# Optimization experiments

Measured on AMD Instinct MI355X. Metric: run time of the kernel, lower is better.

## Reference

```python
import jax, jax.numpy as jnp
import numpy as np

N_NODES = 50000
N_PROP = 25000
N_EDGES = 600000
HIDDEN = 128


def setup_inputs() -> dict:
    key = jax.random.key(0)
    ks = jax.random.split(key, 8)
    prop_z = jax.random.normal(ks[0], (N_NODES, HIDDEN), dtype=jnp.float32)
    mol_z = jax.random.normal(ks[1], (N_NODES, HIDDEN), dtype=jnp.float32)
    # Linear(hidden, hidden) params (y = x @ W.T + b, torch convention)
    W = jax.random.normal(ks[2], (HIDDEN, HIDDEN), dtype=jnp.float32) / np.sqrt(HIDDEN)
    b = jax.random.normal(ks[3], (HIDDEN,), dtype=jnp.float32) * 0.01
    # edges: dst constrained to prop_nodes = [0, N_PROP) so in_edges(prop_nodes) == all edges
    parent_src = jax.random.randint(ks[4], (N_EDGES,), 0, N_NODES, dtype=jnp.int32)
    parent_dst = jax.random.randint(ks[5], (N_EDGES,), 0, N_PROP, dtype=jnp.int32)
    sibling_src = jax.random.randint(ks[6], (N_EDGES,), 0, N_NODES, dtype=jnp.int32)
    sibling_dst = jax.random.randint(ks[7], (N_EDGES,), 0, N_PROP, dtype=jnp.int32)
    prop_nodes = jnp.arange(N_PROP, dtype=jnp.int32)
    return {"prop_z": prop_z, "mol_z": mol_z, "W": W, "b": b,
            "parent_src": parent_src, "parent_dst": parent_dst,
            "sibling_src": sibling_src, "sibling_dst": sibling_dst,
            "prop_nodes": prop_nodes}


def reference(prop_z, mol_z, W, b, parent_src, parent_dst, sibling_src, sibling_dst, prop_nodes):
    n = prop_z.shape[0]
    # parent edges: gather src prop_z, sum into dst (copy_src + sum)
    parent_agg = jax.ops.segment_sum(prop_z[parent_src], parent_dst, num_segments=n)  # [N, H]
    # prop_z[prop_nodes] += relu(linear(parent_prop_z[prop_nodes]))
    upd = jax.nn.relu(parent_agg[prop_nodes] @ W.T + b)  # [P, H]
    prop_z = prop_z.at[prop_nodes].add(upd)
    # sibling edges: gather src mol_z, sum into dst, add at prop_nodes
    sibling_agg = jax.ops.segment_sum(mol_z[sibling_src], sibling_dst, num_segments=n)  # [N, H]
    prop_z = prop_z.at[prop_nodes].add(sibling_agg[prop_nodes])
    return prop_z
```

## Files before the change

kernel.cpp:

```cpp
#include <hip/hip_runtime.h>

#define HIDDEN    128
#define N_NODES_C 50000
#define N_PROP_C  25000
#define N_EDGES_C 600000
#define CAP       64
#define PULL_BLOCKS 6250
#define TAIL_BLOCKS 512
#define GEMV_BLOCKS 1024

__global__ __launch_bounds__(256) void scatter_kernel(
    const int* __restrict__ ps, const int* __restrict__ pd,
    const int* __restrict__ ss, const int* __restrict__ sd,
    int* __restrict__ posP, int* __restrict__ posS,
    int* __restrict__ binP, int* __restrict__ binS)
{
    int i = blockIdx.x * 256 + threadIdx.x;
    if (i < N_EDGES_C) {
        int d = pd[i];
        int r = atomicAdd(&posP[d], 1);
        if (r < CAP) binP[d * CAP + r] = ps[i];
    } else if (i < 2 * N_EDGES_C) {
        int j = i - N_EDGES_C;
        int d = sd[j];
        int r = atomicAdd(&posS[d], 1);
        if (r < CAP) binS[d * CAP + r] = ss[j];
    }
}

__global__ __launch_bounds__(256) void pull_tail_kernel(
    const float* __restrict__ prop_z, const float* __restrict__ mol_z,
    const int* __restrict__ binP, const int* __restrict__ cntP,
    const int* __restrict__ binS, const int* __restrict__ cntS,
    float* __restrict__ aggP, float* __restrict__ aggS,
    float* __restrict__ out)
{
    if (blockIdx.x >= PULL_BLOCKS) {
        const float4* src = (const float4*)(prop_z + (size_t)N_PROP_C * HIDDEN);
        float4*       dst = (float4*)(out + (size_t)N_PROP_C * HIDDEN);
        const int n4 = (N_NODES_C - N_PROP_C) * HIDDEN / 4;
        for (int i = (blockIdx.x - PULL_BLOCKS) * 256 + threadIdx.x; i < n4;
             i += TAIL_BLOCKS * 256)
            dst[i] = src[i];
        return;
    }
    int task = blockIdx.x * 8 + (threadIdx.x >> 5);
    int lane = threadIdx.x & 31;
    const float4* tab; const int* bin; float4* dst; int r, n;
    if (task < N_PROP_C) {
        r = task;            tab = (const float4*)prop_z;
        bin = binP + r * CAP; n = min(cntP[r], CAP); dst = (float4*)aggP;
    } else {
        r = task - N_PROP_C; tab = (const float4*)mol_z;
        bin = binS + r * CAP; n = min(cntS[r], CAP); dst = (float4*)aggS;
    }
    float4 acc = make_float4(0.f, 0.f, 0.f, 0.f);
    int i = 0;
    for (; i + 4 <= n; i += 4) {
        int s0 = bin[i], s1 = bin[i + 1], s2 = bin[i + 2], s3 = bin[i + 3];
        float4 a = tab[s0 * 32 + lane];
        float4 b = tab[s1 * 32 + lane];
        float4 c = tab[s2 * 32 + lane];
        float4 d = tab[s3 * 32 + lane];
        acc.x += (a.x + b.x) + (c.x + d.x);
        acc.y += (a.y + b.y) + (c.y + d.y);
        acc.z += (a.z + b.z) + (c.z + d.z);
        acc.w += (a.w + b.w) + (c.w + d.w);
    }
    for (; i < n; ++i) {
        float4 a = tab[bin[i] * 32 + lane];
        acc.x += a.x; acc.y += a.y; acc.z += a.z; acc.w += a.w;
    }
    dst[r * 32 + lane] = acc;
}

__global__ __launch_bounds__(256) void gemv_out_kernel(
    const float* __restrict__ prop_z,
    const float* __restrict__ aggP, const float* __restrict__ aggS,
    const float* __restrict__ W, const float* __restrict__ bias,
    float* __restrict__ out)
{
    __shared__ float4 Wl[HIDDEN * 32];
    __shared__ float  rowP[8][HIDDEN];
    __shared__ float  rowS[8][HIDDEN];

    const float4* W4 = (const float4*)W;
    for (int i = threadIdx.x; i < HIDDEN * 32; i += 256) {
        int c = i >> 5, k4 = i & 31;
        Wl[(c << 5) | (k4 ^ (c & 31))] = W4[i];
    }
    const int t    = threadIdx.x;
    const int g    = t >> 5;
    const int l4   = t & 31;
    const int c    = t & 127;
    const int half = t >> 7;
    const float bc = bias[c];
    __syncthreads();

    for (int base = blockIdx.x * 8; base < N_PROP_C; base += GEMV_BLOCKS * 8) {
        ((float4*)rowP[g])[l4] = ((const float4*)aggP)[(base + g) * 32 + l4];
        ((float4*)rowS[g])[l4] = ((const float4*)aggS)[(base + g) * 32 + l4];
        __syncthreads();

        const int r0 = half * 4;
        float a0 = bc, a1 = bc, a2 = bc, a3 = bc;
        #pragma unroll
        for (int k4i = 0; k4i < 32; ++k4i) {
            float4 w  = Wl[(c << 5) | (k4i ^ (c & 31))];
            float4 p0 = ((const float4*)rowP[r0 + 0])[k4i];
            float4 p1 = ((const float4*)rowP[r0 + 1])[k4i];
            float4 p2 = ((const float4*)rowP[r0 + 2])[k4i];
            float4 p3 = ((const float4*)rowP[r0 + 3])[k4i];
            a0 = fmaf(w.x, p0.x, fmaf(w.y, p0.y, fmaf(w.z, p0.z, fmaf(w.w, p0.w, a0))));
            a1 = fmaf(w.x, p1.x, fmaf(w.y, p1.y, fmaf(w.z, p1.z, fmaf(w.w, p1.w, a1))));
            a2 = fmaf(w.x, p2.x, fmaf(w.y, p2.y, fmaf(w.z, p2.z, fmaf(w.w, p2.w, a2))));
            a3 = fmaf(w.x, p3.x, fmaf(w.y, p3.y, fmaf(w.z, p3.z, fmaf(w.w, p3.w, a3))));
        }
        float acc[4] = {a0, a1, a2, a3};
        #pragma unroll
        for (int j = 0; j < 4; ++j) {
            int row = base + r0 + j;
            out[(size_t)row * HIDDEN + c] =
                prop_z[(size_t)row * HIDDEN + c] + fmaxf(acc[j], 0.0f)
                + rowS[r0 + j][c];
        }
        __syncthreads();
    }
}

extern "C" void kernel_launch(void* const* d_in, const int* in_sizes, int n_in,
                              void* d_out, int out_size, void* d_ws, size_t ws_size,
                              hipStream_t stream)
{
    const float* prop_z      = (const float*)d_in[0];
    const float* mol_z       = (const float*)d_in[1];
    const float* W           = (const float*)d_in[2];
    const float* b           = (const float*)d_in[3];
    const int*   parent_src  = (const int*)d_in[4];
    const int*   parent_dst  = (const int*)d_in[5];
    const int*   sibling_src = (const int*)d_in[6];
    const int*   sibling_dst = (const int*)d_in[7];

    float* out = (float*)d_out;

    int*   binP = (int*)d_ws;
    int*   binS = binP + (size_t)N_PROP_C * CAP;
    int*   posP = binS + (size_t)N_PROP_C * CAP;
    int*   posS = posP + N_PROP_C;
    float* aggP = (float*)(posS + N_PROP_C);
    float* aggS = aggP + (size_t)N_PROP_C * HIDDEN;

    hipMemsetAsync(posP, 0, 2 * N_PROP_C * sizeof(int), stream);

    int blocks_2e = (2 * N_EDGES_C + 255) / 256;
    scatter_kernel<<<blocks_2e, 256, 0, stream>>>(parent_src, parent_dst,
                                                  sibling_src, sibling_dst,
                                                  posP, posS, binP, binS);

    pull_tail_kernel<<<PULL_BLOCKS + TAIL_BLOCKS, 256, 0, stream>>>(
        prop_z, mol_z, binP, posP, binS, posS, aggP, aggS, out);

    gemv_out_kernel<<<GEMV_BLOCKS, 256, 0, stream>>>(
        prop_z, aggP, aggS, W, b, out);
}
```

Measured before the change: 284.9 us.

## Replace FP32 GEMV epilogue with bf16 MFMA matmul and bf16 parent aggregates

The parent aggregation now stores its result as bf16 instead of fp32. The linear layer is computed with 16x16x32 bf16 MFMA instructions, using W converted to bf16 and held in swizzled shared memory, in place of the scalar FMA GEMV. The pull loop also gains an 8-way unrolled gather to keep more loads in flight. This cuts ALU work and aggregate traffic, at the cost of bf16 rounding error in the matmul inputs, and each block still converts W redundantly.

```diff
diff --git a/kernel.cpp b/kernel.cpp
--- a/kernel.cpp
+++ b/kernel.cpp
@@ -7,7 +7,16 @@
 #define CAP       64
 #define PULL_BLOCKS 6250
 #define TAIL_BLOCKS 512
-#define GEMV_BLOCKS 1024
+#define MFMA_BLOCKS 391
+
+typedef __attribute__((ext_vector_type(8))) short short8;
+typedef __attribute__((ext_vector_type(4))) float f32x4;
+
+__device__ __forceinline__ unsigned short f2bf(float x) {
+    unsigned u = __float_as_uint(x);
+    u += 0x7fffu + ((u >> 16) & 1u);
+    return (unsigned short)(u >> 16);
+}
 
 __global__ __launch_bounds__(256) void scatter_kernel(
     const int* __restrict__ ps, const int* __restrict__ pd,
@@ -32,7 +41,7 @@
     const float* __restrict__ prop_z, const float* __restrict__ mol_z,
     const int* __restrict__ binP, const int* __restrict__ cntP,
     const int* __restrict__ binS, const int* __restrict__ cntS,
-    float* __restrict__ aggP, float* __restrict__ aggS,
+    short* __restrict__ aggPb, float* __restrict__ aggS,
     float* __restrict__ out)
 {
     if (blockIdx.x >= PULL_BLOCKS) {
@@ -46,16 +55,33 @@
     }
     int task = blockIdx.x * 8 + (threadIdx.x >> 5);
     int lane = threadIdx.x & 31;
-    const float4* tab; const int* bin; float4* dst; int r, n;
-    if (task < N_PROP_C) {
+    const float4* tab; const int* bin; int r, n;
+    bool parent = task < N_PROP_C;
+    if (parent) {
         r = task;            tab = (const float4*)prop_z;
-        bin = binP + r * CAP; n = min(cntP[r], CAP); dst = (float4*)aggP;
+        bin = binP + r * CAP; n = min(cntP[r], CAP);
     } else {
         r = task - N_PROP_C; tab = (const float4*)mol_z;
-        bin = binS + r * CAP; n = min(cntS[r], CAP); dst = (float4*)aggS;
+        bin = binS + r * CAP; n = min(cntS[r], CAP);
     }
     float4 acc = make_float4(0.f, 0.f, 0.f, 0.f);
     int i = 0;
+    for (; i + 8 <= n; i += 8) {
+        int s0 = bin[i],     s1 = bin[i + 1], s2 = bin[i + 2], s3 = bin[i + 3];
+        int s4 = bin[i + 4], s5 = bin[i + 5], s6 = bin[i + 6], s7 = bin[i + 7];
+        float4 a = tab[s0 * 32 + lane];
+        float4 b = tab[s1 * 32 + lane];
+        float4 c = tab[s2 * 32 + lane];
+        float4 d = tab[s3 * 32 + lane];
+        float4 e = tab[s4 * 32 + lane];
+        float4 f = tab[s5 * 32 + lane];
+        float4 g = tab[s6 * 32 + lane];
+        float4 h = tab[s7 * 32 + lane];
+        acc.x += ((a.x + b.x) + (c.x + d.x)) + ((e.x + f.x) + (g.x + h.x));
+        acc.y += ((a.y + b.y) + (c.y + d.y)) + ((e.y + f.y) + (g.y + h.y));
+        acc.z += ((a.z + b.z) + (c.z + d.z)) + ((e.z + f.z) + (g.z + h.z));
+        acc.w += ((a.w + b.w) + (c.w + d.w)) + ((e.w + f.w) + (g.w + h.w));
+    }
     for (; i + 4 <= n; i += 4) {
         int s0 = bin[i], s1 = bin[i + 1], s2 = bin[i + 2], s3 = bin[i + 3];
         float4 a = tab[s0 * 32 + lane];
@@ -71,60 +97,72 @@
         float4 a = tab[bin[i] * 32 + lane];
         acc.x += a.x; acc.y += a.y; acc.z += a.z; acc.w += a.w;
     }
-    dst[r * 32 + lane] = acc;
-}
-
-__global__ __launch_bounds__(256) void gemv_out_kernel(
+    if (parent) {
+        ushort4 p;
+        p.x = f2bf(acc.x); p.y = f2bf(acc.y); p.z = f2bf(acc.z); p.w = f2bf(acc.w);
+        *(ushort4*)(aggPb + (size_t)r * HIDDEN + lane * 4) = p;
+    } else {
+        ((float4*)aggS)[r * 32 + lane] = acc;
+    }
+}
+
+__global__ __launch_bounds__(256) void mfma_out_kernel(
     const float* __restrict__ prop_z,
-    const float* __restrict__ aggP, const float* __restrict__ aggS,
+    const short* __restrict__ aggPb, const float* __restrict__ aggS,
     const float* __restrict__ W, const float* __restrict__ bias,
     float* __restrict__ out)
 {
-    __shared__ float4 Wl[HIDDEN * 32];
-    __shared__ float  rowP[8][HIDDEN];
-    __shared__ float  rowS[8][HIDDEN];
+    __shared__ __align__(16) short Wb[HIDDEN * HIDDEN];
 
     const float4* W4 = (const float4*)W;
-    for (int i = threadIdx.x; i < HIDDEN * 32; i += 256) {
-        int c = i >> 5, k4 = i & 31;
-        Wl[(c << 5) | (k4 ^ (c & 31))] = W4[i];
-    }
-    const int t    = threadIdx.x;
-    const int g    = t >> 5;
-    const int l4   = t & 31;
-    const int c    = t & 127;
-    const int half = t >> 7;
-    const float bc = bias[c];
+    for (int ch = threadIdx.x; ch < HIDDEN * HIDDEN / 8; ch += 256) {
+        int c = ch >> 4, kb = ch & 15;
+        float4 w0 = W4[ch * 2], w1 = W4[ch * 2 + 1];
+        short8 s;
+        s[0] = (short)f2bf(w0.x); s[1] = (short)f2bf(w0.y);
+        s[2] = (short)f2bf(w0.z); s[3] = (short)f2bf(w0.w);
+        s[4] = (short)f2bf(w1.x); s[5] = (short)f2bf(w1.y);
+        s[6] = (short)f2bf(w1.z); s[7] = (short)f2bf(w1.w);
+        ((short8*)Wb)[c * 16 + (kb ^ (c & 15))] = s;
+    }
     __syncthreads();
 
-    for (int base = blockIdx.x * 8; base < N_PROP_C; base += GEMV_BLOCKS * 8) {
-        ((float4*)rowP[g])[l4] = ((const float4*)aggP)[(base + g) * 32 + l4];
-        ((float4*)rowS[g])[l4] = ((const float4*)aggS)[(base + g) * 32 + l4];
-        __syncthreads();
-
-        const int r0 = half * 4;
-        float a0 = bc, a1 = bc, a2 = bc, a3 = bc;
+    int task = blockIdx.x * 4 + (threadIdx.x >> 6);
+    int r0 = task * 16;
+    if (r0 >= N_PROP_C) return;
+    int lane = threadIdx.x & 63;
+    int arow = r0 + (lane & 15);
+    int aoff = (lane >> 4) * 8;
+
+    f32x4 acc[8] = {};
+    #pragma unroll
+    for (int ks = 0; ks < 4; ++ks) {
+        int k0 = ks * 32 + aoff;
+        short8 a = {};
+        if (arow < N_PROP_C)
+            a = *(const short8*)(aggPb + (size_t)arow * HIDDEN + k0);
+        int kb = ks * 4 + (lane >> 4);
         #pragma unroll
-        for (int k4i = 0; k4i < 32; ++k4i) {
-            float4 w  = Wl[(c << 5) | (k4i ^ (c & 31))];
-            float4 p0 = ((const float4*)rowP[r0 + 0])[k4i];
-            float4 p1 = ((const float4*)rowP[r0 + 1])[k4i];
-            float4 p2 = ((const float4*)rowP[r0 + 2])[k4i];
-            float4 p3 = ((const float4*)rowP[r0 + 3])[k4i];
-            a0 = fmaf(w.x, p0.x, fmaf(w.y, p0.y, fmaf(w.z, p0.z, fmaf(w.w, p0.w, a0))));
-            a1 = fmaf(w.x, p1.x, fmaf(w.y, p1.y, fmaf(w.z, p1.z, fmaf(w.w, p1.w, a1))));
-            a2 = fmaf(w.x, p2.x, fmaf(w.y, p2.y, fmaf(w.z, p2.z, fmaf(w.w, p2.w, a2))));
-            a3 = fmaf(w.x, p3.x, fmaf(w.y, p3.y, fmaf(w.z, p3.z, fmaf(w.w, p3.w, a3))));
+        for (int ct = 0; ct < 8; ++ct) {
+            int c = ct * 16 + (lane & 15);
+            short8 b = ((const short8*)Wb)[c * 16 + (kb ^ (c & 15))];
+            acc[ct] = __builtin_amdgcn_mfma_f32_16x16x32_bf16(a, b, acc[ct], 0, 0, 0);
         }
-        float acc[4] = {a0, a1, a2, a3};
+    }
+
+    int rl = (lane >> 4) * 4;
+    #pragma unroll
+    for (int ct = 0; ct < 8; ++ct) {
+        int col = ct * 16 + (lane & 15);
+        float bc = bias[col];
         #pragma unroll
-        for (int j = 0; j < 4; ++j) {
-            int row = base + r0 + j;
-            out[(size_t)row * HIDDEN + c] =
-                prop_z[(size_t)row * HIDDEN + c] + fmaxf(acc[j], 0.0f)
-                + rowS[r0 + j][c];
+        for (int r = 0; r < 4; ++r) {
+            int row = r0 + rl + r;
+            if (row < N_PROP_C) {
+                size_t idx = (size_t)row * HIDDEN + col;
+                out[idx] = prop_z[idx] + fmaxf(acc[ct][r] + bc, 0.0f) + aggS[idx];
+            }
         }
-        __syncthreads();
     }
 }
 
@@ -143,12 +181,12 @@
 
     float* out = (float*)d_out;
 
-    int*   binP = (int*)d_ws;
-    int*   binS = binP + (size_t)N_PROP_C * CAP;
-    int*   posP = binS + (size_t)N_PROP_C * CAP;
-    int*   posS = posP + N_PROP_C;
-    float* aggP = (float*)(posS + N_PROP_C);
-    float* aggS = aggP + (size_t)N_PROP_C * HIDDEN;
+    int*   binP  = (int*)d_ws;
+    int*   binS  = binP + (size_t)N_PROP_C * CAP;
+    int*   posP  = binS + (size_t)N_PROP_C * CAP;
+    int*   posS  = posP + N_PROP_C;
+    short* aggPb = (short*)(posS + N_PROP_C);
+    float* aggS  = (float*)(aggPb + (size_t)N_PROP_C * HIDDEN);
 
     hipMemsetAsync(posP, 0, 2 * N_PROP_C * sizeof(int), stream);
 
@@ -158,8 +196,8 @@
                                                   posP, posS, binP, binS);
 
     pull_tail_kernel<<<PULL_BLOCKS + TAIL_BLOCKS, 256, 0, stream>>>(
-        prop_z, mol_z, binP, posP, binS, posS, aggP, aggS, out);
-
-    gemv_out_kernel<<<GEMV_BLOCKS, 256, 0, stream>>>(
-        prop_z, aggP, aggS, W, b, out);
-}
+        prop_z, mol_z, binP, posP, binS, posS, aggPb, aggS, out);
+
+    mfma_out_kernel<<<MFMA_BLOCKS, 256, 0, stream>>>(
+        prop_z, aggPb, aggS, W, b, out);
+}
```

Result: faster. 261.7 us (-8.2%).
